# Kernel tuning notes

Hardware: AMD Instinct MI355X
Metric: run time of the kernel (lower is better)

Reference implementation:

```python
import jax, jax.numpy as jnp
import numpy as np

L, D, H, DH, FF, V, B, T, WD, BAND = 4, 512, 8, 64, 2048, 32000, 2, 1024, 32, 128
SCALE = 1.0 / float(np.sqrt(DH))

# per-head causal masks: even heads full causal, odd heads banded causal (0 <= i-j < BAND)
_diff = np.arange(T)[:, None] - np.arange(T)[None, :]
_full = _diff >= 0
_band = _full & (_diff < BAND)
MASKS = jnp.asarray(np.where((np.arange(H) % 2 == 0)[:, None, None], _full, _band))  # (H,T,T) bool
# ALiBi slopes for H=8 (power of 2): start=ratio=2^(-2^(-(log2(8)-3)))=0.5 -> 0.5^(1..8)
_slopes = 0.5 ** np.arange(1, H + 1)
ALIBI = jnp.asarray((-_slopes[:, None, None] * _diff).astype(np.float32))  # (H,T,T)


def _ln(x, g, b):
    m = x.mean(-1, keepdims=True)
    v = ((x - m) ** 2).mean(-1, keepdims=True)
    return (x - m) / jnp.sqrt(v + 1e-5) * g + b


def setup_inputs() -> dict:
    key = jax.random.key(0)
    ks = jax.random.split(key, 16)
    s = 0.02
    n = lambda k, shape: jax.random.normal(k, shape, jnp.float32) * s
    return dict(
        idx=jax.random.randint(ks[0], (B, T), 0, V),
        wte=n(ks[1], (V, D)), wpe=n(ks[2], (T, D)),
        ln1_g=jnp.ones((L, D)), ln1_b=jnp.zeros((L, D)),
        attn_w=n(ks[3], (L, 3 * D, D)), attn_b=jnp.zeros((L, 3 * D)),
        proj_w=n(ks[4], (L, D, D)), proj_b=jnp.zeros((L, D)),
        dape_gw=n(ks[5], (L, WD, 2 * H)), dape_gb=jnp.zeros((L, WD)),
        dape_vw=n(ks[6], (L, WD, 2 * H)), dape_vb=jnp.zeros((L, WD)),
        dape_ow=n(ks[7], (L, H, WD)), dape_ob=jnp.zeros((L, H)),
        ln2_g=jnp.ones((L, D)), ln2_b=jnp.zeros((L, D)),
        gate_w=n(ks[8], (L, FF, D)), gate_b=jnp.zeros((L, FF)),
        val_w=n(ks[9], (L, FF, D)), val_b=jnp.zeros((L, FF)),
        mlp_w=n(ks[10], (L, D, FF)), mlp_b=jnp.zeros((L, D)),
        lnf_g=jnp.ones((D,)), lnf_b=jnp.zeros((D,)),
        lm_w=n(ks[11], (V, D)),
    )


def reference(idx, wte, wpe, ln1_g, ln1_b, attn_w, attn_b, proj_w, proj_b,
              dape_gw, dape_gb, dape_vw, dape_vb, dape_ow, dape_ob,
              ln2_g, ln2_b, gate_w, gate_b, val_w, val_b, mlp_w, mlp_b,
              lnf_g, lnf_b, lm_w):
    x = wte[idx] + wpe[jnp.arange(T)][None]  # (B,T,D)
    for l in range(L):
        h = _ln(x, ln1_g[l], ln1_b[l])
        qkv = h @ attn_w[l].T + attn_b[l]
        q, k, v = jnp.split(qkv, 3, axis=-1)
        q = q.reshape(B, T, H, DH).transpose(0, 2, 1, 3)
        k = k.reshape(B, T, H, DH).transpose(0, 2, 1, 3)
        v = v.reshape(B, T, H, DH).transpose(0, 2, 1, 3)
        att = jnp.einsum('bhqd,bhkd->bhqk', q, k) * SCALE  # (B,H,T,T)
        # DAPE: concat(att, zero base bias) along head dim, pointwise SWIGLU MLP 2H->WD->H
        cat = jnp.concatenate([att, jnp.zeros_like(att)], axis=1).transpose(0, 2, 3, 1)  # (B,T,T,2H)
        hid = jax.nn.silu(cat @ dape_gw[l].T + dape_gb[l]) * (cat @ dape_vw[l].T + dape_vb[l])
        lb = hid @ dape_ow[l].T + dape_ob[l]  # (B,T,T,H)
        att = att + lb.transpose(0, 3, 1, 2) + ALIBI[None]
        att = jnp.where(MASKS[None], att, -jnp.inf)
        att = jax.nn.softmax(att, axis=-1)
        y = jnp.einsum('bhqk,bhkd->bhqd', att, v).transpose(0, 2, 1, 3).reshape(B, T, D)
        x = x + y @ proj_w[l].T + proj_b[l]
        h2 = _ln(x, ln2_g[l], ln2_b[l])
        ff = jax.nn.silu(h2 @ gate_w[l].T + gate_b[l]) * (h2 @ val_w[l].T + val_b[l])
        x = x + ff @ mlp_w[l].T + mlp_b[l]
    x = _ln(x, lnf_g, lnf_b)
    return x @ lm_w.T  # (B,T,V)
```

## Files before the change

### kernel.cpp

```cpp
#include <hip/hip_runtime.h>
#include <hip/hip_bf16.h>
#include <math.h>

constexpr int L = 4, D = 512, H = 8, DH = 64, FF = 2048, V = 32000, B = 2, T = 1024, WD = 32, BAND = 128;
constexpr float SCALE = 0.125f;

typedef __hip_bfloat16 bf16;
typedef __attribute__((ext_vector_type(8))) short short8;
typedef __attribute__((ext_vector_type(4))) float floatx4;

#define MFMA16(a, b, c) __builtin_amdgcn_mfma_f32_16x16x32_bf16(a, b, c, 0, 0, 0)

__device__ inline void gl_lds16(const void* g, void* l) {
    __builtin_amdgcn_global_load_lds((const __attribute__((address_space(1))) unsigned int*)g,
                                     (__attribute__((address_space(3))) unsigned int*)l, 16, 0, 0);
}

__global__ __launch_bounds__(256) void embed_k(const int* __restrict__ idx,
                                               const float* __restrict__ wte,
                                               const float* __restrict__ wpe,
                                               float* __restrict__ x) {
    int row = blockIdx.x;
    int t = row % T;
    int token = idx[row];
    const float* we = wte + (size_t)token * D;
    const float* pe = wpe + (size_t)t * D;
    float* xo = x + (size_t)row * D;
    for (int d = threadIdx.x; d < D; d += 256) xo[d] = we[d] + pe[d];
}

__global__ __launch_bounds__(256) void f2b_k(const float* __restrict__ in,
                                             bf16* __restrict__ out, int n4) {
    int i = blockIdx.x * 256 + threadIdx.x;
    if (i >= n4) return;
    float4 v = *(const float4*)&in[(size_t)i * 4];
    bf16 o[4] = {__float2bfloat16(v.x), __float2bfloat16(v.y),
                 __float2bfloat16(v.z), __float2bfloat16(v.w)};
    *(ulong1*)&out[(size_t)i * 4] = *(ulong1*)o;
}

__global__ __launch_bounds__(256) void ln_bf16_k(const float* __restrict__ x,
                                                 const float* __restrict__ g,
                                                 const float* __restrict__ b,
                                                 bf16* __restrict__ o) {
    int row = blockIdx.x;
    const float* xr = x + (size_t)row * D;
    int d0 = threadIdx.x, d1 = threadIdx.x + 256;
    float v0 = xr[d0], v1 = xr[d1];
    float s = v0 + v1, ss = v0 * v0 + v1 * v1;
    for (int off = 32; off > 0; off >>= 1) {
        s  += __shfl_down(s, off);
        ss += __shfl_down(ss, off);
    }
    __shared__ float red[2][4];
    int wid = threadIdx.x >> 6;
    if ((threadIdx.x & 63) == 0) { red[0][wid] = s; red[1][wid] = ss; }
    __syncthreads();
    s  = red[0][0] + red[0][1] + red[0][2] + red[0][3];
    ss = red[1][0] + red[1][1] + red[1][2] + red[1][3];
    float mean = s * (1.0f / D);
    float var  = ss * (1.0f / D) - mean * mean;
    float rstd = rsqrtf(var + 1e-5f);
    bf16* orow = o + (size_t)row * D;
    orow[d0] = __float2bfloat16((v0 - mean) * rstd * g[d0] + b[d0]);
    orow[d1] = __float2bfloat16((v1 - mean) * rstd * g[d1] + b[d1]);
}

template <int BM, int BN, int EPI>
__global__ __launch_bounds__(256) void mgemm_k(const bf16* __restrict__ A,
                                               const bf16* __restrict__ W,
                                               const float* __restrict__ bias,
                                               const float* res,
                                               float* C, int M, int N, int K) {
    constexpr int WM = BM / 2, WN = BN / 2;
    constexpr int FM = WM / 16, FN = WN / 16;
    constexpr int CA = BM / 64, CB = BN / 64;
    __shared__ __align__(16) bf16 As[BM * 32];
    __shared__ __align__(16) bf16 Bs[BN * 32];
    int tid = threadIdx.x;
    int wave = tid >> 6, lane = tid & 63;
    int quad = lane >> 4, l16 = lane & 15;
    int m0 = blockIdx.y * BM, n0 = blockIdx.x * BN;
    int wm = wave >> 1, wn = wave & 1;
    floatx4 acc[FM][FN] = {};

    const bf16* Ag[CA];
    const bf16* Wg[CB];
    bf16* lA[CA];
    bf16* lB[CB];
#pragma unroll
    for (int c = 0; c < CA; c++) {
        int idx = c * 256 + tid;
        Ag[c] = A + (size_t)(m0 + (idx >> 2)) * K + (idx & 3) * 8;
        lA[c] = As + (size_t)(c * 256 + wave * 64) * 8;
    }
#pragma unroll
    for (int c = 0; c < CB; c++) {
        int idx = c * 256 + tid;
        Wg[c] = W + (size_t)(n0 + (idx >> 2)) * K + (idx & 3) * 8;
        lB[c] = Bs + (size_t)(c * 256 + wave * 64) * 8;
    }

    for (int k0 = 0; k0 < K; k0 += 32) {
        __syncthreads();
#pragma unroll
        for (int c = 0; c < CA; c++) gl_lds16(Ag[c] + k0, lA[c]);
#pragma unroll
        for (int c = 0; c < CB; c++) gl_lds16(Wg[c] + k0, lB[c]);
        __syncthreads();
        short8 a[FM], b[FN];
#pragma unroll
        for (int mi = 0; mi < FM; mi++)
            a[mi] = *(const short8*)&As[(wm * WM + mi * 16 + l16) * 32 + quad * 8];
#pragma unroll
        for (int ni = 0; ni < FN; ni++)
            b[ni] = *(const short8*)&Bs[(wn * WN + ni * 16 + l16) * 32 + quad * 8];
#pragma unroll
        for (int mi = 0; mi < FM; mi++)
#pragma unroll
            for (int ni = 0; ni < FN; ni++)
                acc[mi][ni] = MFMA16(a[mi], b[ni], acc[mi][ni]);
    }

    int row_base = m0 + wm * WM + quad * 4;
    int col_base = n0 + wn * WN + l16;
#pragma unroll
    for (int mi = 0; mi < FM; mi++) {
#pragma unroll
        for (int r = 0; r < 4; r++) {
            int m = row_base + mi * 16 + r;
#pragma unroll
            for (int ni = 0; ni < FN; ni++) {
                int n = col_base + ni * 16;
                float v = acc[mi][ni][r];
                if (EPI == 0 || EPI == 1 || EPI == 3) v += bias[n];
                if (EPI == 1) v += res[(size_t)m * N + n];
                if (EPI == 3) {
                    ((bf16*)C)[(size_t)m * N + n] = __float2bfloat16(v);
                } else {
                    C[(size_t)m * N + n] = v;
                }
            }
        }
    }
}

__global__ __launch_bounds__(256) void mgemm_glu_k(const bf16* __restrict__ A,
                                                   const bf16* __restrict__ Wgp,
                                                   const bf16* __restrict__ Wvp,
                                                   const float* __restrict__ gbias,
                                                   const float* __restrict__ vbias,
                                                   bf16* __restrict__ O,
                                                   int M, int N, int K) {
    constexpr int BM = 128, BN = 64, WM = 64, WN = 32, FM = 4, FN = 2;
    __shared__ __align__(16) bf16 As[BM * 32];
    __shared__ __align__(16) bf16 Gs[BN * 32];
    __shared__ __align__(16) bf16 Vs[BN * 32];
    int tid = threadIdx.x;
    int wave = tid >> 6, lane = tid & 63;
    int quad = lane >> 4, l16 = lane & 15;
    int m0 = blockIdx.y * BM, n0 = blockIdx.x * BN;
    int wm = wave >> 1, wn = wave & 1;
    floatx4 accg[FM][FN] = {}, accv[FM][FN] = {};

    int idx0 = tid, idx1 = tid + 256;
    const bf16* Ag0 = A + (size_t)(m0 + (idx0 >> 2)) * K + (idx0 & 3) * 8;
    const bf16* Ag1 = A + (size_t)(m0 + (idx1 >> 2)) * K + (idx1 & 3) * 8;
    const bf16* Gg = Wgp + (size_t)(n0 + (idx0 >> 2)) * K + (idx0 & 3) * 8;
    const bf16* Vg = Wvp + (size_t)(n0 + (idx0 >> 2)) * K + (idx0 & 3) * 8;
    bf16* lA0 = As + (size_t)(wave * 64) * 8;
    bf16* lA1 = As + (size_t)(256 + wave * 64) * 8;
    bf16* lG = Gs + (size_t)(wave * 64) * 8;
    bf16* lV = Vs + (size_t)(wave * 64) * 8;

    for (int k0 = 0; k0 < K; k0 += 32) {
        __syncthreads();
        gl_lds16(Ag0 + k0, lA0);
        gl_lds16(Ag1 + k0, lA1);
        gl_lds16(Gg + k0, lG);
        gl_lds16(Vg + k0, lV);
        __syncthreads();
        short8 a[FM], g[FN], v[FN];
#pragma unroll
        for (int mi = 0; mi < FM; mi++)
            a[mi] = *(const short8*)&As[(wm * WM + mi * 16 + l16) * 32 + quad * 8];
#pragma unroll
        for (int ni = 0; ni < FN; ni++) {
            g[ni] = *(const short8*)&Gs[(wn * WN + ni * 16 + l16) * 32 + quad * 8];
            v[ni] = *(const short8*)&Vs[(wn * WN + ni * 16 + l16) * 32 + quad * 8];
        }
#pragma unroll
        for (int mi = 0; mi < FM; mi++)
#pragma unroll
            for (int ni = 0; ni < FN; ni++) {
                accg[mi][ni] = MFMA16(a[mi], g[ni], accg[mi][ni]);
                accv[mi][ni] = MFMA16(a[mi], v[ni], accv[mi][ni]);
            }
    }

    int row_base = m0 + wm * WM + quad * 4;
    int col_base = n0 + wn * WN + l16;
#pragma unroll
    for (int mi = 0; mi < FM; mi++) {
#pragma unroll
        for (int r = 0; r < 4; r++) {
            int m = row_base + mi * 16 + r;
#pragma unroll
            for (int ni = 0; ni < FN; ni++) {
                int n = col_base + ni * 16;
                float gv = accg[mi][ni][r] + gbias[n];
                float vv = accv[mi][ni][r] + vbias[n];
                float o = gv / (1.0f + __expf(-gv)) * vv;
                O[(size_t)m * N + n] = __float2bfloat16(o);
            }
        }
    }
}

__global__ __launch_bounds__(256) void vt_k(const bf16* __restrict__ qkvb,
                                            bf16* __restrict__ vT) {
    int bh = blockIdx.y, b = bh >> 3, h = bh & 7;
    int t0 = blockIdx.x * 64;
    __shared__ bf16 Ls[64][72];
    int tid = threadIdx.x;
#pragma unroll
    for (int it = 0; it < 2; it++) {
        int c = it * 256 + tid;
        int r = c >> 3, s = c & 7;
        *(short8*)&Ls[r][s * 8] =
            *(const short8*)&qkvb[((size_t)(b * T + t0 + r)) * (3 * D) + 2 * D + h * DH + s * 8];
    }
    __syncthreads();
    int d = tid & 63;
    int tg = tid >> 6;
    for (int k = tg; k < 8; k += 4) {
        union { unsigned short u[8]; short8 v; } tmp;
#pragma unroll
        for (int e = 0; e < 8; e++) tmp.u[e] = *(const unsigned short*)&Ls[k * 8 + e][d];
        *(short8*)&vT[((size_t)bh * DH + d) * T + t0 + k * 8] = tmp.v;
    }
}

__global__ __launch_bounds__(256) void qk_mfma_k(const bf16* __restrict__ qkvb,
                                                 float* __restrict__ att) {
    int bh = blockIdx.z; int b = bh >> 3, h = bh & 7;
    int i0 = blockIdx.y * 64, j0 = blockIdx.x * 64;
    if (j0 > i0 + 63) return;
    __shared__ __align__(16) bf16 Qs[64 * 64];
    __shared__ __align__(16) bf16 Ks[64 * 64];
    int tid = threadIdx.x;
    int wave = tid >> 6, lane = tid & 63;
    int l16 = lane & 15, quad = lane >> 4;
    int wi = wave >> 1, wj = wave & 1;

    const bf16* Qbase = qkvb + ((size_t)(b * T + i0)) * (3 * D) + h * DH;
    const bf16* Kbase = qkvb + ((size_t)(b * T + j0)) * (3 * D) + D + h * DH;
#pragma unroll
    for (int it = 0; it < 2; it++) {
        int cbase = it * 256 + wave * 64;
        int c = cbase + lane;
        int r = c >> 3, s = c & 7, gs = s ^ (r & 7);
        gl_lds16(Qbase + (size_t)r * (3 * D) + gs * 8, Qs + (size_t)cbase * 8);
        gl_lds16(Kbase + (size_t)r * (3 * D) + gs * 8, Ks + (size_t)cbase * 8);
    }
    __syncthreads();

    floatx4 acc[2][2] = {};
#pragma unroll
    for (int ks = 0; ks < 2; ks++) {
        short8 a[2], bb[2];
#pragma unroll
        for (int mi = 0; mi < 2; mi++) {
            int row = wi * 32 + mi * 16 + l16;
            a[mi] = *(const short8*)&Qs[row * 64 + (((ks * 4 + quad) ^ (row & 7)) * 8)];
        }
#pragma unroll
        for (int ni = 0; ni < 2; ni++) {
            int row = wj * 32 + ni * 16 + l16;
            bb[ni] = *(const short8*)&Ks[row * 64 + (((ks * 4 + quad) ^ (row & 7)) * 8)];
        }
#pragma unroll
        for (int mi = 0; mi < 2; mi++)
#pragma unroll
            for (int ni = 0; ni < 2; ni++)
                acc[mi][ni] = MFMA16(a[mi], bb[ni], acc[mi][ni]);
    }

    size_t obase = ((size_t)bh * T + (i0 + wi * 32)) * T + (j0 + wj * 32);
#pragma unroll
    for (int mi = 0; mi < 2; mi++)
#pragma unroll
        for (int r = 0; r < 4; r++)
#pragma unroll
            for (int ni = 0; ni < 2; ni++)
                att[obase + (size_t)(mi * 16 + quad * 4 + r) * T + ni * 16 + l16] =
                    acc[mi][ni][r] * SCALE;
}

__global__ __launch_bounds__(256) void dape_sm_k(const float* __restrict__ att,
                                                 bf16* __restrict__ P,
                                                 const float* __restrict__ gw,
                                                 const float* __restrict__ gb,
                                                 const float* __restrict__ vw,
                                                 const float* __restrict__ vb,
                                                 const float* __restrict__ ow,
                                                 const float* __restrict__ ob) {
    int bi = blockIdx.x;
    int b = bi >> 10;
    int i = (T - 1) - (bi & (T - 1));
    int tid = threadIdx.x;
    int wave = tid >> 6, lane = tid & 63;

    __shared__ float4 sgw[WD][2], svw[WD][2], sow[WD][2];
    __shared__ float sgb[WD], svb[WD], sob[H];
    __shared__ float redm[4][8], reds[4][8];
    if (tid < WD) {
        sgw[tid][0] = *(const float4*)&gw[tid * 2 * H];
        sgw[tid][1] = *(const float4*)&gw[tid * 2 * H + 4];
        svw[tid][0] = *(const float4*)&vw[tid * 2 * H];
        svw[tid][1] = *(const float4*)&vw[tid * 2 * H + 4];
        sgb[tid] = gb[tid]; svb[tid] = vb[tid];
        float o0[4], o1[4];
#pragma unroll
        for (int hh = 0; hh < 4; hh++) o0[hh] = ow[hh * WD + tid];
#pragma unroll
        for (int hh = 0; hh < 4; hh++) o1[hh] = ow[(hh + 4) * WD + tid];
        sow[tid][0] = *(float4*)o0;
        sow[tid][1] = *(float4*)o1;
    }
    if (tid < H) sob[tid] = ob[tid];
    __syncthreads();

    const float slopes[8] = {0.5f, 0.25f, 0.125f, 0.0625f,
                             0.03125f, 0.015625f, 0.0078125f, 0.00390625f};
    size_t abase = (size_t)b * H * T * T + (size_t)i * T;

    float sv[4][8];
    int jv[4];
#pragma unroll
    for (int c = 0; c < 4; c++) {
        int j = tid + c * 256;
        jv[c] = j;
        if (j <= i) {
#pragma unroll
            for (int hh = 0; hh < 8; hh++)
                sv[c][hh] = att[abase + (size_t)hh * T * T + j];
        }
    }

    float lb[4][8];
#pragma unroll
    for (int c = 0; c < 4; c++)
#pragma unroll
        for (int hh = 0; hh < 8; hh++) lb[c][hh] = sob[hh];
    for (int w = 0; w < WD; w++) {
        float4 g0 = sgw[w][0], g1 = sgw[w][1];
        float4 v0 = svw[w][0], v1 = svw[w][1];
        float4 o0 = sow[w][0], o1 = sow[w][1];
        float gbb = sgb[w], vbb = svb[w];
#pragma unroll
        for (int c = 0; c < 4; c++) {
            if (jv[c] <= i) {
                float g = gbb + sv[c][0] * g0.x + sv[c][1] * g0.y + sv[c][2] * g0.z + sv[c][3] * g0.w
                              + sv[c][4] * g1.x + sv[c][5] * g1.y + sv[c][6] * g1.z + sv[c][7] * g1.w;
                float v = vbb + sv[c][0] * v0.x + sv[c][1] * v0.y + sv[c][2] * v0.z + sv[c][3] * v0.w
                              + sv[c][4] * v1.x + sv[c][5] * v1.y + sv[c][6] * v1.z + sv[c][7] * v1.w;
                float hid = g / (1.0f + __expf(-g)) * v;
                lb[c][0] += hid * o0.x; lb[c][1] += hid * o0.y;
                lb[c][2] += hid * o0.z; lb[c][3] += hid * o0.w;
                lb[c][4] += hid * o1.x; lb[c][5] += hid * o1.y;
                lb[c][6] += hid * o1.z; lb[c][7] += hid * o1.w;
            }
        }
    }

    float mx[8];
#pragma unroll
    for (int hh = 0; hh < 8; hh++) mx[hh] = -1e30f;
#pragma unroll
    for (int c = 0; c < 4; c++) {
        if (jv[c] <= i) {
            float diff = (float)(i - jv[c]);
#pragma unroll
            for (int hh = 0; hh < 8; hh++) {
                float val = sv[c][hh] + lb[c][hh] - slopes[hh] * diff;
                if ((hh & 1) && (jv[c] < i - (BAND - 1))) val = -1e30f;
                sv[c][hh] = val;
                mx[hh] = fmaxf(mx[hh], val);
            }
        }
    }
    for (int off = 32; off > 0; off >>= 1)
#pragma unroll
        for (int hh = 0; hh < 8; hh++) mx[hh] = fmaxf(mx[hh], __shfl_down(mx[hh], off));
    if (lane == 0)
#pragma unroll
        for (int hh = 0; hh < 8; hh++) redm[wave][hh] = mx[hh];
    __syncthreads();
#pragma unroll
    for (int hh = 0; hh < 8; hh++)
        mx[hh] = fmaxf(fmaxf(redm[0][hh], redm[1][hh]), fmaxf(redm[2][hh], redm[3][hh]));

    float sm[8];
#pragma unroll
    for (int hh = 0; hh < 8; hh++) sm[hh] = 0.f;
#pragma unroll
    for (int c = 0; c < 4; c++) {
        if (jv[c] <= i) {
#pragma unroll
            for (int hh = 0; hh < 8; hh++) {
                float p = __expf(sv[c][hh] - mx[hh]);
                sv[c][hh] = p;
                sm[hh] += p;
            }
        }
    }
    for (int off = 32; off > 0; off >>= 1)
#pragma unroll
        for (int hh = 0; hh < 8; hh++) sm[hh] += __shfl_down(sm[hh], off);
    if (lane == 0)
#pragma unroll
        for (int hh = 0; hh < 8; hh++) reds[wave][hh] = sm[hh];
    __syncthreads();
    float inv[8];
#pragma unroll
    for (int hh = 0; hh < 8; hh++)
        inv[hh] = 1.0f / (reds[0][hh] + reds[1][hh] + reds[2][hh] + reds[3][hh]);

    size_t pbase = (size_t)b * H * T * T + (size_t)i * T;
#pragma unroll
    for (int c = 0; c < 4; c++) {
        if (jv[c] <= i) {
#pragma unroll
            for (int hh = 0; hh < 8; hh++)
                P[pbase + (size_t)hh * T * T + jv[c]] = __float2bfloat16(sv[c][hh] * inv[hh]);
        }
    }
    int ia = i & ~63;
    int zhi = ia + 63;
    for (int j = i + 1 + tid; j <= zhi; j += 256)
#pragma unroll
        for (int hh = 0; hh < 8; hh++)
            P[pbase + (size_t)hh * T * T + j] = __float2bfloat16(0.f);
    int js = (ia - (BAND - 1) > 0 ? ia - (BAND - 1) : 0) & ~31;
    for (int j = js + tid; j <= i - BAND; j += 256)
#pragma unroll
        for (int hh = 1; hh < 8; hh += 2)
            P[pbase + (size_t)hh * T * T + j] = __float2bfloat16(0.f);
}

__global__ __launch_bounds__(256) void av_mfma_k(const bf16* __restrict__ P,
                                                 const bf16* __restrict__ vT,
                                                 bf16* __restrict__ y) {
    int bh = blockIdx.y; int b = bh >> 3, h = bh & 7;
    int ia = blockIdx.x * 64;
    __shared__ __align__(16) bf16 Ps[64 * 32];
    __shared__ __align__(16) bf16 Vs[64 * 32];
    int tid = threadIdx.x, wave = tid >> 6, lane = tid & 63;
    int l16 = lane & 15, quad = lane >> 4;
    int wi = wave >> 1, wn = wave & 1;
    floatx4 acc[2][2] = {};

    int j_end = ia + 63;
    int j_start = (h & 1) ? ((ia - (BAND - 1) > 0 ? ia - (BAND - 1) : 0) & ~31) : 0;
    const bf16* Pbase = P + ((size_t)bh * T + ia) * T;
    const bf16* Vbase = vT + (size_t)bh * DH * T;
    int r = tid >> 2, s = tid & 3, gs = s ^ ((r >> 1) & 3);
    bf16* lP = Ps + (size_t)(wave * 64) * 8;
    bf16* lV = Vs + (size_t)(wave * 64) * 8;

    for (int j0 = j_start; j0 <= j_end; j0 += 32) {
        __syncthreads();
        gl_lds16(Pbase + (size_t)r * T + j0 + gs * 8, lP);
        gl_lds16(Vbase + (size_t)r * T + j0 + gs * 8, lV);
        __syncthreads();
        short8 a[2], bb[2];
#pragma unroll
        for (int mi = 0; mi < 2; mi++) {
            int row = wi * 32 + mi * 16 + l16;
            a[mi] = *(const short8*)&Ps[row * 32 + ((quad ^ ((row >> 1) & 3)) * 8)];
        }
#pragma unroll
        for (int ni = 0; ni < 2; ni++) {
            int row = wn * 32 + ni * 16 + l16;
            bb[ni] = *(const short8*)&Vs[row * 32 + ((quad ^ ((row >> 1) & 3)) * 8)];
        }
#pragma unroll
        for (int mi = 0; mi < 2; mi++)
#pragma unroll
            for (int ni = 0; ni < 2; ni++)
                acc[mi][ni] = MFMA16(a[mi], bb[ni], acc[mi][ni]);
    }

#pragma unroll
    for (int mi = 0; mi < 2; mi++)
#pragma unroll
        for (int rr = 0; rr < 4; rr++) {
            int i = ia + wi * 32 + mi * 16 + quad * 4 + rr;
#pragma unroll
            for (int ni = 0; ni < 2; ni++) {
                int d = wn * 32 + ni * 16 + l16;
                y[((size_t)(b * T + i)) * D + h * DH + d] = __float2bfloat16(acc[mi][ni][rr]);
            }
        }
}

extern "C" void kernel_launch(void* const* d_in, const int* in_sizes, int n_in,
                              void* d_out, int out_size, void* d_ws, size_t ws_size,
                              hipStream_t stream) {
    const int*   idx     = (const int*)d_in[0];
    const float* wte     = (const float*)d_in[1];
    const float* wpe     = (const float*)d_in[2];
    const float* ln1_g   = (const float*)d_in[3];
    const float* ln1_b   = (const float*)d_in[4];
    const float* attn_w  = (const float*)d_in[5];
    const float* attn_b  = (const float*)d_in[6];
    const float* proj_w  = (const float*)d_in[7];
    const float* proj_b  = (const float*)d_in[8];
    const float* dape_gw = (const float*)d_in[9];
    const float* dape_gb = (const float*)d_in[10];
    const float* dape_vw = (const float*)d_in[11];
    const float* dape_vb = (const float*)d_in[12];
    const float* dape_ow = (const float*)d_in[13];
    const float* dape_ob = (const float*)d_in[14];
    const float* ln2_g   = (const float*)d_in[15];
    const float* ln2_b   = (const float*)d_in[16];
    const float* gate_w  = (const float*)d_in[17];
    const float* gate_b  = (const float*)d_in[18];
    const float* val_w   = (const float*)d_in[19];
    const float* val_b   = (const float*)d_in[20];
    const float* mlp_w   = (const float*)d_in[21];
    const float* mlp_b   = (const float*)d_in[22];
    const float* lnf_g   = (const float*)d_in[23];
    const float* lnf_b   = (const float*)d_in[24];
    const float* lm_w    = (const float*)d_in[25];
    float* out = (float*)d_out;

    float* ws   = (float*)d_ws;
    float* x    = ws;
    float* att  = x + (size_t)B * T * D;
    bf16*  hb   = (bf16*)(att + (size_t)B * H * T * T);
    bf16*  yb   = hb   + (size_t)B * T * D;
    bf16*  ffb  = yb   + (size_t)B * T * D;
    bf16*  qkvb = ffb  + (size_t)B * T * FF;
    bf16*  vTb  = qkvb + (size_t)B * T * 3 * D;
    bf16*  Pb   = vTb  + (size_t)B * H * DH * T;
    bf16*  wq   = Pb   + (size_t)B * H * T * T;
    bf16*  wp   = wq   + (size_t)L * 3 * D * D;
    bf16*  wg   = wp   + (size_t)L * D * D;
    bf16*  wv   = wg   + (size_t)L * FF * D;
    bf16*  wm   = wv   + (size_t)L * FF * D;
    bf16*  wl   = wm   + (size_t)L * D * FF;

    auto conv = [&](const float* src, bf16* dst, size_t n) {
        int n4 = (int)(n / 4);
        f2b_k<<<(n4 + 255) / 256, 256, 0, stream>>>(src, dst, n4);
    };
    conv(attn_w, wq, (size_t)L * 3 * D * D);
    conv(proj_w, wp, (size_t)L * D * D);
    conv(gate_w, wg, (size_t)L * FF * D);
    conv(val_w,  wv, (size_t)L * FF * D);
    conv(mlp_w,  wm, (size_t)L * D * FF);
    conv(lm_w,   wl, (size_t)V * D);

    embed_k<<<B * T, 256, 0, stream>>>(idx, wte, wpe, x);

    const int M = B * T;
    for (int l = 0; l < L; l++) {
        ln_bf16_k<<<M, 256, 0, stream>>>(x, ln1_g + l * D, ln1_b + l * D, hb);
        mgemm_k<128, 64, 3><<<dim3(3 * D / 64, M / 128), 256, 0, stream>>>(
            hb, wq + (size_t)l * 3 * D * D, attn_b + l * 3 * D, nullptr, (float*)qkvb, M, 3 * D, D);
        vt_k<<<dim3(T / 64, B * H), 256, 0, stream>>>(qkvb, vTb);
        qk_mfma_k<<<dim3(T / 64, T / 64, B * H), 256, 0, stream>>>(qkvb, att);
        dape_sm_k<<<B * T, 256, 0, stream>>>(att, Pb,
            dape_gw + l * WD * 2 * H, dape_gb + l * WD,
            dape_vw + l * WD * 2 * H, dape_vb + l * WD,
            dape_ow + l * H * WD, dape_ob + l * H);
        av_mfma_k<<<dim3(T / 64, B * H), 256, 0, stream>>>(Pb, vTb, yb);
        mgemm_k<128, 64, 1><<<dim3(D / 64, M / 128), 256, 0, stream>>>(
            yb, wp + (size_t)l * D * D, proj_b + l * D, x, x, M, D, D);
        ln_bf16_k<<<M, 256, 0, stream>>>(x, ln2_g + l * D, ln2_b + l * D, hb);
        mgemm_glu_k<<<dim3(FF / 64, M / 128), 256, 0, stream>>>(
            hb, wg + (size_t)l * FF * D, wv + (size_t)l * FF * D,
            gate_b + l * FF, val_b + l * FF, ffb, M, FF, D);
        mgemm_k<128, 64, 1><<<dim3(D / 64, M / 128), 256, 0, stream>>>(
            ffb, wm + (size_t)l * D * FF, mlp_b + l * D, x, x, M, D, FF);
    }

    ln_bf16_k<<<M, 256, 0, stream>>>(x, lnf_g, lnf_b, hb);
    mgemm_k<128, 128, 2><<<dim3(V / 128, M / 128), 256, 0, stream>>>(
        hb, wl, nullptr, nullptr, out, M, V, D);
}
```

Measured before the change: 1.327 ms.

## Double-buffer LDS tiles with XOR swizzle in GEMM and AV kernels

Adds double-buffered shared-memory staging to the generic GEMM, the gated GEMM and the attention-value kernel, so the global-to-LDS load of the next K tile overlaps MFMA work on the current one, with one barrier per iteration instead of two. It also applies an XOR swizzle to LDS chunk placement to cut bank conflicts, and raises the generic GEMM K-tile to 64. The LM-head GEMM switches from 128x128 to 128x64 tiles. These changes double the LDS footprint per block, which may lower occupancy, and the prefetch relies on the global_load_lds completing before the end-of-iteration barrier.

```diff
diff --git a/kernel.cpp b/kernel.cpp
--- a/kernel.cpp
+++ b/kernel.cpp
@@ -66,7 +66,7 @@
     orow[d1] = __float2bfloat16((v1 - mean) * rstd * g[d1] + b[d1]);
 }
 
-template <int BM, int BN, int EPI>
+template <int BM, int BN, int BK, int EPI>
 __global__ __launch_bounds__(256) void mgemm_k(const bf16* __restrict__ A,
                                                const bf16* __restrict__ W,
                                                const float* __restrict__ bias,
@@ -74,9 +74,11 @@
                                                float* C, int M, int N, int K) {
     constexpr int WM = BM / 2, WN = BN / 2;
     constexpr int FM = WM / 16, FN = WN / 16;
-    constexpr int CA = BM / 64, CB = BN / 64;
-    __shared__ __align__(16) bf16 As[BM * 32];
-    __shared__ __align__(16) bf16 Bs[BN * 32];
+    constexpr int RCH = BK / 8;
+    constexpr int CA = BM * RCH / 256, CB = BN * RCH / 256;
+    constexpr int KS = BK / 32;
+    __shared__ __align__(16) bf16 As[2][BM * BK];
+    __shared__ __align__(16) bf16 Bs[2][BN * BK];
     int tid = threadIdx.x;
     int wave = tid >> 6, lane = tid & 63;
     int quad = lane >> 4, l16 = lane & 15;
@@ -86,40 +88,57 @@
 
     const bf16* Ag[CA];
     const bf16* Wg[CB];
-    bf16* lA[CA];
-    bf16* lB[CB];
 #pragma unroll
     for (int c = 0; c < CA; c++) {
-        int idx = c * 256 + tid;
-        Ag[c] = A + (size_t)(m0 + (idx >> 2)) * K + (idx & 3) * 8;
-        lA[c] = As + (size_t)(c * 256 + wave * 64) * 8;
+        int idx = c * 256 + tid, r = idx / RCH, s = idx % RCH;
+        int gs = (RCH == 8) ? (s ^ (r & 7)) : (s ^ ((r >> 1) & 3));
+        Ag[c] = A + (size_t)(m0 + r) * K + gs * 8;
     }
 #pragma unroll
     for (int c = 0; c < CB; c++) {
-        int idx = c * 256 + tid;
-        Wg[c] = W + (size_t)(n0 + (idx >> 2)) * K + (idx & 3) * 8;
-        lB[c] = Bs + (size_t)(c * 256 + wave * 64) * 8;
-    }
-
-    for (int k0 = 0; k0 < K; k0 += 32) {
+        int idx = c * 256 + tid, r = idx / RCH, s = idx % RCH;
+        int gs = (RCH == 8) ? (s ^ (r & 7)) : (s ^ ((r >> 1) & 3));
+        Wg[c] = W + (size_t)(n0 + r) * K + gs * 8;
+    }
+    int ldsoff = wave * 64 * 8;
+
+#pragma unroll
+    for (int c = 0; c < CA; c++) gl_lds16(Ag[c], &As[0][c * 2048 + ldsoff]);
+#pragma unroll
+    for (int c = 0; c < CB; c++) gl_lds16(Wg[c], &Bs[0][c * 2048 + ldsoff]);
+    __syncthreads();
+
+    int p = 0;
+    for (int k0 = 0; k0 < K; k0 += BK) {
+        if (k0 + BK < K) {
+#pragma unroll
+            for (int c = 0; c < CA; c++) gl_lds16(Ag[c] + k0 + BK, &As[p ^ 1][c * 2048 + ldsoff]);
+#pragma unroll
+            for (int c = 0; c < CB; c++) gl_lds16(Wg[c] + k0 + BK, &Bs[p ^ 1][c * 2048 + ldsoff]);
+        }
+#pragma unroll
+        for (int ksub = 0; ksub < KS; ksub++) {
+            short8 a[FM], b[FN];
+#pragma unroll
+            for (int mi = 0; mi < FM; mi++) {
+                int row = wm * WM + mi * 16 + l16;
+                int cc = (ksub * 4 + quad) ^ ((RCH == 8) ? (row & 7) : ((row >> 1) & 3));
+                a[mi] = *(const short8*)&As[p][row * BK + cc * 8];
+            }
+#pragma unroll
+            for (int ni = 0; ni < FN; ni++) {
+                int row = wn * WN + ni * 16 + l16;
+                int cc = (ksub * 4 + quad) ^ ((RCH == 8) ? (row & 7) : ((row >> 1) & 3));
+                b[ni] = *(const short8*)&Bs[p][row * BK + cc * 8];
+            }
+#pragma unroll
+            for (int mi = 0; mi < FM; mi++)
+#pragma unroll
+                for (int ni = 0; ni < FN; ni++)
+                    acc[mi][ni] = MFMA16(a[mi], b[ni], acc[mi][ni]);
+        }
         __syncthreads();
-#pragma unroll
-        for (int c = 0; c < CA; c++) gl_lds16(Ag[c] + k0, lA[c]);
-#pragma unroll
-        for (int c = 0; c < CB; c++) gl_lds16(Wg[c] + k0, lB[c]);
-        __syncthreads();
-        short8 a[FM], b[FN];
-#pragma unroll
-        for (int mi = 0; mi < FM; mi++)
-            a[mi] = *(const short8*)&As[(wm * WM + mi * 16 + l16) * 32 + quad * 8];
-#pragma unroll
-        for (int ni = 0; ni < FN; ni++)
-            b[ni] = *(const short8*)&Bs[(wn * WN + ni * 16 + l16) * 32 + quad * 8];
-#pragma unroll
-        for (int mi = 0; mi < FM; mi++)
-#pragma unroll
-            for (int ni = 0; ni < FN; ni++)
-                acc[mi][ni] = MFMA16(a[mi], b[ni], acc[mi][ni]);
+        p ^= 1;
     }
 
     int row_base = m0 + wm * WM + quad * 4;
@@ -153,9 +172,9 @@
                                                    bf16* __restrict__ O,
                                                    int M, int N, int K) {
     constexpr int BM = 128, BN = 64, WM = 64, WN = 32, FM = 4, FN = 2;
-    __shared__ __align__(16) bf16 As[BM * 32];
-    __shared__ __align__(16) bf16 Gs[BN * 32];
-    __shared__ __align__(16) bf16 Vs[BN * 32];
+    __shared__ __align__(16) bf16 As[2][BM * 32];
+    __shared__ __align__(16) bf16 Gs[2][BN * 32];
+    __shared__ __align__(16) bf16 Vs[2][BN * 32];
     int tid = threadIdx.x;
     int wave = tid >> 6, lane = tid & 63;
     int quad = lane >> 4, l16 = lane & 15;
@@ -163,31 +182,50 @@
     int wm = wave >> 1, wn = wave & 1;
     floatx4 accg[FM][FN] = {}, accv[FM][FN] = {};
 
-    int idx0 = tid, idx1 = tid + 256;
-    const bf16* Ag0 = A + (size_t)(m0 + (idx0 >> 2)) * K + (idx0 & 3) * 8;
-    const bf16* Ag1 = A + (size_t)(m0 + (idx1 >> 2)) * K + (idx1 & 3) * 8;
-    const bf16* Gg = Wgp + (size_t)(n0 + (idx0 >> 2)) * K + (idx0 & 3) * 8;
-    const bf16* Vg = Wvp + (size_t)(n0 + (idx0 >> 2)) * K + (idx0 & 3) * 8;
-    bf16* lA0 = As + (size_t)(wave * 64) * 8;
-    bf16* lA1 = As + (size_t)(256 + wave * 64) * 8;
-    bf16* lG = Gs + (size_t)(wave * 64) * 8;
-    bf16* lV = Vs + (size_t)(wave * 64) * 8;
-
+    const bf16* Ag[2];
+#pragma unroll
+    for (int c = 0; c < 2; c++) {
+        int idx = c * 256 + tid, r = idx >> 2, s = idx & 3;
+        int gs = s ^ ((r >> 1) & 3);
+        Ag[c] = A + (size_t)(m0 + r) * K + gs * 8;
+    }
+    const bf16* Gg;
+    const bf16* Vg;
+    {
+        int r = tid >> 2, s = tid & 3;
+        int gs = s ^ ((r >> 1) & 3);
+        Gg = Wgp + (size_t)(n0 + r) * K + gs * 8;
+        Vg = Wvp + (size_t)(n0 + r) * K + gs * 8;
+    }
+    int ldsoff = wave * 64 * 8;
+
+#pragma unroll
+    for (int c = 0; c < 2; c++) gl_lds16(Ag[c], &As[0][c * 2048 + ldsoff]);
+    gl_lds16(Gg, &Gs[0][ldsoff]);
+    gl_lds16(Vg, &Vs[0][ldsoff]);
+    __syncthreads();
+
+    int p = 0;
     for (int k0 = 0; k0 < K; k0 += 32) {
-        __syncthreads();
-        gl_lds16(Ag0 + k0, lA0);
-        gl_lds16(Ag1 + k0, lA1);
-        gl_lds16(Gg + k0, lG);
-        gl_lds16(Vg + k0, lV);
-        __syncthreads();
+        if (k0 + 32 < K) {
+#pragma unroll
+            for (int c = 0; c < 2; c++) gl_lds16(Ag[c] + k0 + 32, &As[p ^ 1][c * 2048 + ldsoff]);
+            gl_lds16(Gg + k0 + 32, &Gs[p ^ 1][ldsoff]);
+            gl_lds16(Vg + k0 + 32, &Vs[p ^ 1][ldsoff]);
+        }
         short8 a[FM], g[FN], v[FN];
 #pragma unroll
-        for (int mi = 0; mi < FM; mi++)
-            a[mi] = *(const short8*)&As[(wm * WM + mi * 16 + l16) * 32 + quad * 8];
+        for (int mi = 0; mi < FM; mi++) {
+            int row = wm * WM + mi * 16 + l16;
+            int cc = quad ^ ((row >> 1) & 3);
+            a[mi] = *(const short8*)&As[p][row * 32 + cc * 8];
+        }
 #pragma unroll
         for (int ni = 0; ni < FN; ni++) {
-            g[ni] = *(const short8*)&Gs[(wn * WN + ni * 16 + l16) * 32 + quad * 8];
-            v[ni] = *(const short8*)&Vs[(wn * WN + ni * 16 + l16) * 32 + quad * 8];
+            int row = wn * WN + ni * 16 + l16;
+            int cc = quad ^ ((row >> 1) & 3);
+            g[ni] = *(const short8*)&Gs[p][row * 32 + cc * 8];
+            v[ni] = *(const short8*)&Vs[p][row * 32 + cc * 8];
         }
 #pragma unroll
         for (int mi = 0; mi < FM; mi++)
@@ -196,6 +234,8 @@
                 accg[mi][ni] = MFMA16(a[mi], g[ni], accg[mi][ni]);
                 accv[mi][ni] = MFMA16(a[mi], v[ni], accv[mi][ni]);
             }
+        __syncthreads();
+        p ^= 1;
     }
 
     int row_base = m0 + wm * WM + quad * 4;
@@ -454,8 +494,8 @@
                                                  bf16* __restrict__ y) {
     int bh = blockIdx.y; int b = bh >> 3, h = bh & 7;
     int ia = blockIdx.x * 64;
-    __shared__ __align__(16) bf16 Ps[64 * 32];
-    __shared__ __align__(16) bf16 Vs[64 * 32];
+    __shared__ __align__(16) bf16 Ps[2][64 * 32];
+    __shared__ __align__(16) bf16 Vs[2][64 * 32];
     int tid = threadIdx.x, wave = tid >> 6, lane = tid & 63;
     int l16 = lane & 15, quad = lane >> 4;
     int wi = wave >> 1, wn = wave & 1;
@@ -466,30 +506,36 @@
     const bf16* Pbase = P + ((size_t)bh * T + ia) * T;
     const bf16* Vbase = vT + (size_t)bh * DH * T;
     int r = tid >> 2, s = tid & 3, gs = s ^ ((r >> 1) & 3);
-    bf16* lP = Ps + (size_t)(wave * 64) * 8;
-    bf16* lV = Vs + (size_t)(wave * 64) * 8;
-
+    int ldsoff = wave * 64 * 8;
+
+    gl_lds16(Pbase + (size_t)r * T + j_start + gs * 8, &Ps[0][ldsoff]);
+    gl_lds16(Vbase + (size_t)r * T + j_start + gs * 8, &Vs[0][ldsoff]);
+    __syncthreads();
+
+    int p = 0;
     for (int j0 = j_start; j0 <= j_end; j0 += 32) {
-        __syncthreads();
-        gl_lds16(Pbase + (size_t)r * T + j0 + gs * 8, lP);
-        gl_lds16(Vbase + (size_t)r * T + j0 + gs * 8, lV);
-        __syncthreads();
+        if (j0 + 32 <= j_end) {
+            gl_lds16(Pbase + (size_t)r * T + j0 + 32 + gs * 8, &Ps[p ^ 1][ldsoff]);
+            gl_lds16(Vbase + (size_t)r * T + j0 + 32 + gs * 8, &Vs[p ^ 1][ldsoff]);
+        }
         short8 a[2], bb[2];
 #pragma unroll
         for (int mi = 0; mi < 2; mi++) {
             int row = wi * 32 + mi * 16 + l16;
-            a[mi] = *(const short8*)&Ps[row * 32 + ((quad ^ ((row >> 1) & 3)) * 8)];
+            a[mi] = *(const short8*)&Ps[p][row * 32 + ((quad ^ ((row >> 1) & 3)) * 8)];
         }
 #pragma unroll
         for (int ni = 0; ni < 2; ni++) {
             int row = wn * 32 + ni * 16 + l16;
-            bb[ni] = *(const short8*)&Vs[row * 32 + ((quad ^ ((row >> 1) & 3)) * 8)];
+            bb[ni] = *(const short8*)&Vs[p][row * 32 + ((quad ^ ((row >> 1) & 3)) * 8)];
         }
 #pragma unroll
         for (int mi = 0; mi < 2; mi++)
 #pragma unroll
             for (int ni = 0; ni < 2; ni++)
                 acc[mi][ni] = MFMA16(a[mi], bb[ni], acc[mi][ni]);
+        __syncthreads();
+        p ^= 1;
     }
 
 #pragma unroll
@@ -568,7 +614,7 @@
     const int M = B * T;
     for (int l = 0; l < L; l++) {
         ln_bf16_k<<<M, 256, 0, stream>>>(x, ln1_g + l * D, ln1_b + l * D, hb);
-        mgemm_k<128, 64, 3><<<dim3(3 * D / 64, M / 128), 256, 0, stream>>>(
+        mgemm_k<128, 64, 64, 3><<<dim3(3 * D / 64, M / 128), 256, 0, stream>>>(
             hb, wq + (size_t)l * 3 * D * D, attn_b + l * 3 * D, nullptr, (float*)qkvb, M, 3 * D, D);
         vt_k<<<dim3(T / 64, B * H), 256, 0, stream>>>(qkvb, vTb);
         qk_mfma_k<<<dim3(T / 64, T / 64, B * H), 256, 0, stream>>>(qkvb, att);
@@ -577,17 +623,17 @@
             dape_vw + l * WD * 2 * H, dape_vb + l * WD,
             dape_ow + l * H * WD, dape_ob + l * H);
         av_mfma_k<<<dim3(T / 64, B * H), 256, 0, stream>>>(Pb, vTb, yb);
-        mgemm_k<128, 64, 1><<<dim3(D / 64, M / 128), 256, 0, stream>>>(
+        mgemm_k<128, 64, 64, 1><<<dim3(D / 64, M / 128), 256, 0, stream>>>(
             yb, wp + (size_t)l * D * D, proj_b + l * D, x, x, M, D, D);
         ln_bf16_k<<<M, 256, 0, stream>>>(x, ln2_g + l * D, ln2_b + l * D, hb);
         mgemm_glu_k<<<dim3(FF / 64, M / 128), 256, 0, stream>>>(
             hb, wg + (size_t)l * FF * D, wv + (size_t)l * FF * D,
             gate_b + l * FF, val_b + l * FF, ffb, M, FF, D);
-        mgemm_k<128, 64, 1><<<dim3(D / 64, M / 128), 256, 0, stream>>>(
+        mgemm_k<128, 64, 64, 1><<<dim3(D / 64, M / 128), 256, 0, stream>>>(
             ffb, wm + (size_t)l * D * FF, mlp_b + l * D, x, x, M, D, FF);
     }
 
     ln_bf16_k<<<M, 256, 0, stream>>>(x, lnf_g, lnf_b, hb);
-    mgemm_k<128, 128, 2><<<dim3(V / 128, M / 128), 256, 0, stream>>>(
+    mgemm_k<128, 64, 64, 2><<<dim3(V / 64, M / 128), 256, 0, stream>>>(
         hb, wl, nullptr, nullptr, out, M, V, D);
 }
```

Result: faster. 1.283 ms (-3.3%).
